# Kernel tuning notes

Measured on AMD Instinct MI355X. Metric: run time of the kernel, lower is better.

Reference implementation:

```python
import jax, jax.numpy as jnp
import numpy as np

GRID = 300  # NaiveFourierKANLayer default gridsize
EPS = 1e-5


def layer_norm(x, w, b):
    mu = jnp.mean(x, axis=-1, keepdims=True)
    var = jnp.var(x, axis=-1, keepdims=True)
    return (x - mu) * jax.lax.rsqrt(var + EPS) * w + b


def fourier_kan(x, coeffs, bias):
    # x: [..., I], coeffs: [2, O, I, G], bias: [1, O]
    shp = x.shape
    I = shp[-1]
    xf = x.reshape(-1, I)
    k = jnp.arange(1, GRID + 1, dtype=x.dtype)           # [G]
    arg = xf[:, :, None] * k                             # [B, I, G]
    y = jnp.einsum('big,oig->bo', jnp.cos(arg), coeffs[0])
    y = y + jnp.einsum('big,oig->bo', jnp.sin(arg), coeffs[1])
    y = y + bias                                         # bias broadcasts [1, O]
    return y.reshape(shp[:-1] + (coeffs.shape[1],))


def setup_inputs() -> dict:
    key = jax.random.key(0)
    ks = jax.random.split(key, 4)
    B, N, D = 8, 196, 128          # batch, in_channels, in_dim
    O1 = 2 * D                     # amplifier out_dim
    x = jax.random.normal(ks[0], (B, N, D), dtype=jnp.float32)
    fc1_coeffs = jax.random.normal(ks[1], (2, O1, D, GRID), dtype=jnp.float32) / np.sqrt(D * GRID)
    fc2_coeffs = jax.random.normal(ks[2], (2, N, N, GRID), dtype=jnp.float32) / np.sqrt(N * GRID)
    return {
        'x': x,
        'ln1_w': jnp.ones((D,), jnp.float32),
        'ln1_b': jnp.zeros((D,), jnp.float32),
        'fc1_coeffs': fc1_coeffs,
        'fc1_bias': jnp.zeros((1, O1), jnp.float32),
        'ln2_w': jnp.ones((O1,), jnp.float32),
        'ln2_b': jnp.zeros((O1,), jnp.float32),
        'fc2_coeffs': fc2_coeffs,
        'fc2_bias': jnp.zeros((1, N), jnp.float32),
    }


def reference(x, ln1_w, ln1_b, fc1_coeffs, fc1_bias, ln2_w, ln2_b, fc2_coeffs, fc2_bias):
    B, N, D = x.shape
    # amplifier: LN over in_dim, FourierKAN in_dim -> 2*in_dim
    h = fourier_kan(layer_norm(x, ln1_w, ln1_b), fc1_coeffs, fc1_bias)   # [B, N, 2D]
    # channel_mix: LN over 2*in_dim, transpose, FourierKAN over channels, transpose back
    h = layer_norm(h, ln2_w, ln2_b)
    h = jnp.transpose(h, (0, 2, 1))                                      # [B, 2D, N]
    h = fourier_kan(h, fc2_coeffs, fc2_bias)                             # [B, 2D, N]
    h = jnp.transpose(h, (0, 2, 1))                                      # [B, N, 2D]
    return h.reshape(-1, 2 * N, D)                                       # [B, 2N, D]
```

## Files before the change

### kernel.cpp

```cpp
#include <hip/hip_runtime.h>
#include <math.h>

typedef short short8 __attribute__((ext_vector_type(8)));
typedef float f32x4 __attribute__((ext_vector_type(4)));

#define EPSF 1e-5f

union FragU { uint4 q; unsigned u[4]; short8 v; };

__device__ __forceinline__ unsigned pack_trunc2(float lo_val, float hi_val) {
    return __builtin_amdgcn_perm(__float_as_uint(hi_val), __float_as_uint(lo_val), 0x07060302u);
}
__device__ __forceinline__ float trunc_bf(float x) {
    return __uint_as_float(__float_as_uint(x) & 0xFFFF0000u);
}

#define LGKM0_BAR() do { \
    asm volatile("s_waitcnt lgkmcnt(0)" ::: "memory"); \
    __builtin_amdgcn_s_barrier(); \
    __builtin_amdgcn_sched_barrier(0); \
    asm volatile("" ::: "memory"); \
} while (0)

__global__ void ln1_kernel(const float* __restrict__ x, const float* __restrict__ w,
                           const float* __restrict__ b, float* __restrict__ xnT) {
    int r = blockIdx.x;
    int t = threadIdx.x;
    const float* row = x + (size_t)r * 128;
    float v0 = row[t], v1 = row[t + 64];
    float s = v0 + v1, q = v0 * v0 + v1 * v1;
    #pragma unroll
    for (int off = 32; off > 0; off >>= 1) {
        s += __shfl_down(s, off);
        q += __shfl_down(q, off);
    }
    s = __shfl(s, 0); q = __shfl(q, 0);
    float mu = s * (1.f / 128.f);
    float var = q * (1.f / 128.f) - mu * mu;
    float rs = rsqrtf(var + EPSF);
    xnT[(size_t)t * 1792 + r]        = (v0 - mu) * rs * w[t]      + b[t];
    xnT[(size_t)(t + 64) * 1792 + r] = (v1 - mu) * rs * w[t + 64] + b[t + 64];
}

__launch_bounds__(256)
__global__ void fc1_kernel(const float* __restrict__ xnT, const float* __restrict__ coeffs,
                           float* __restrict__ h1, int KS) {
    const int nt = blockIdx.x;
    const int mt = blockIdx.y;
    const int ks = blockIdx.z;
    const int i0 = (ks * 128) / KS, i1 = ((ks + 1) * 128) / KS;
    const int t = threadIdx.x;
    const int wv = t >> 6, ln = t & 63;
    const int q = ln >> 4, col = ln & 15;
    const int mwrow = mt * 256 + wv * 64;

    __shared__ unsigned bhi[128 * 36];
    __shared__ unsigned blo[128 * 36];

    const float* c0 = coeffs;
    const float* c1 = coeffs + (size_t)256 * 128 * 300;

    f32x4 acc[4][8] = {};

    const int srow = t >> 1;
    const int j0 = (t & 1) * 16;
    const int og = nt * 128 + srow;
    const size_t prow = (size_t)og * 128;

    for (int i = i0; i < i1; ++i) {
        float zu[4];
        #pragma unroll
        for (int mf = 0; mf < 4; ++mf) {
            int m = mwrow + mf * 16 + col;
            zu[mf] = (m < 1568) ? xnT[(size_t)i * 1792 + m] : 0.f;
        }
        const float* p0 = c0 + (prow + i) * 300;
        const float* p1 = c1 + (prow + i) * 300;

        for (int c = 0; c < 10; ++c) {
            __syncthreads();
            {
                unsigned hw[16], lw[16];
                #pragma unroll
                for (int k4 = 0; k4 < 4; ++k4) {
                    int g = c * 32 + j0 + k4 * 4;
                    float w0[4], w1[4];
                    if (g + 4 <= 300) {
                        float4 a = *(const float4*)(p0 + g);
                        float4 bb = *(const float4*)(p1 + g);
                        w0[0]=a.x; w0[1]=a.y; w0[2]=a.z; w0[3]=a.w;
                        w1[0]=bb.x; w1[1]=bb.y; w1[2]=bb.z; w1[3]=bb.w;
                    } else {
                        #pragma unroll
                        for (int e = 0; e < 4; ++e) {
                            int gg = g + e; bool ok = gg < 300;
                            w0[e] = ok ? p0[gg] : 0.f;
                            w1[e] = ok ? p1[gg] : 0.f;
                        }
                    }
                    #pragma unroll
                    for (int e = 0; e < 4; ++e) {
                        hw[k4*4+e] = pack_trunc2(w0[e], w1[e]);
                        lw[k4*4+e] = pack_trunc2(w0[e]-trunc_bf(w0[e]), w1[e]-trunc_bf(w1[e]));
                    }
                }
                int base = srow * 36 + j0;
                *(uint4*)&bhi[base]      = make_uint4(hw[0], hw[1], hw[2], hw[3]);
                *(uint4*)&bhi[base + 4]  = make_uint4(hw[4], hw[5], hw[6], hw[7]);
                *(uint4*)&bhi[base + 8]  = make_uint4(hw[8], hw[9], hw[10], hw[11]);
                *(uint4*)&bhi[base + 12] = make_uint4(hw[12], hw[13], hw[14], hw[15]);
                *(uint4*)&blo[base]      = make_uint4(lw[0], lw[1], lw[2], lw[3]);
                *(uint4*)&blo[base + 4]  = make_uint4(lw[4], lw[5], lw[6], lw[7]);
                *(uint4*)&blo[base + 8]  = make_uint4(lw[8], lw[9], lw[10], lw[11]);
                *(uint4*)&blo[base + 12] = make_uint4(lw[12], lw[13], lw[14], lw[15]);
            }
            __syncthreads();
            #pragma unroll
            for (int h = 0; h < 2; ++h) {
                FragU ah[4], al[4];
                #pragma unroll
                for (int mf = 0; mf < 4; ++mf) {
                    #pragma unroll
                    for (int d = 0; d < 4; ++d) {
                        float kf = (float)(c * 32 + h * 16 + q * 4 + d + 1);
                        float a = zu[mf] * kf;
                        float cv = __cosf(a), sv = __sinf(a);
                        ah[mf].u[d] = pack_trunc2(cv, sv);
                        al[mf].u[d] = pack_trunc2(cv - trunc_bf(cv), sv - trunc_bf(sv));
                    }
                }
                #pragma unroll
                for (int nf = 0; nf < 8; ++nf) {
                    int addr = (nf * 16 + col) * 36 + h * 16 + q * 4;
                    FragU bh, bl;
                    bh.q = *(const uint4*)&bhi[addr];
                    bl.q = *(const uint4*)&blo[addr];
                    #pragma unroll
                    for (int mf = 0; mf < 4; ++mf) {
                        acc[mf][nf] = __builtin_amdgcn_mfma_f32_16x16x32_bf16(ah[mf].v, bh.v, acc[mf][nf], 0, 0, 0);
                        acc[mf][nf] = __builtin_amdgcn_mfma_f32_16x16x32_bf16(ah[mf].v, bl.v, acc[mf][nf], 0, 0, 0);
                        acc[mf][nf] = __builtin_amdgcn_mfma_f32_16x16x32_bf16(al[mf].v, bh.v, acc[mf][nf], 0, 0, 0);
                    }
                }
            }
        }
    }
    #pragma unroll
    for (int mf = 0; mf < 4; ++mf) {
        if (mwrow + mf * 16 >= 1568) continue;
        int mbase = mwrow + mf * 16 + q * 4;
        #pragma unroll
        for (int nf = 0; nf < 8; ++nf) {
            int o = nt * 128 + nf * 16 + col;
            #pragma unroll
            for (int r = 0; r < 4; ++r)
                atomicAdd(&h1[(size_t)(mbase + r) * 256 + o], acc[mf][nf][r]);
        }
    }
}

__global__ void ln2_kernel(const float* __restrict__ h1, const float* __restrict__ bias,
                           const float* __restrict__ w, const float* __restrict__ b,
                           float* __restrict__ h1n) {
    int r = blockIdx.x;
    int t = threadIdx.x;
    float v = h1[(size_t)r * 256 + t] + bias[t];
    float s = v, q = v * v;
    #pragma unroll
    for (int off = 32; off > 0; off >>= 1) {
        s += __shfl_down(s, off);
        q += __shfl_down(q, off);
    }
    __shared__ float ss[4], qq[4];
    int wid = t >> 6;
    if ((t & 63) == 0) { ss[wid] = s; qq[wid] = q; }
    __syncthreads();
    float S = ss[0] + ss[1] + ss[2] + ss[3];
    float Q = qq[0] + qq[1] + qq[2] + qq[3];
    float mu = S * (1.f / 256.f);
    float var = Q * (1.f / 256.f) - mu * mu;
    float rs = rsqrtf(var + EPSF);
    h1n[(size_t)r * 256 + t] = (v - mu) * rs * w[t] + b[t];
}

__device__ __forceinline__ void cmul(float& xr, float& xi, float br, float bi) {
    float nr = xr * br - xi * bi;
    float ni = xr * bi + xi * br;
    xr = nr; xi = ni;
}

__launch_bounds__(256)
__global__ void fc2_kernel(const float* __restrict__ h1n, const float* __restrict__ coeffs,
                           float* __restrict__ out, int KS) {
    const int nt = blockIdx.x;
    const int b  = blockIdx.y;
    const int ks = blockIdx.z;
    const int i0 = (ks * 196) / KS, i1 = ((ks + 1) * 196) / KS;
    const int t = threadIdx.x;
    const int wv = t >> 6, ln = t & 63;
    const int q = ln >> 4, col = ln & 15;
    const int cwb = wv * 64;

    __shared__ unsigned bs[2][128 * 36];

    const float* d0 = coeffs;
    const float* d1 = coeffs + (size_t)196 * 196 * 300;

    f32x4 acc[4][8] = {};

    const int srow = t >> 1;
    const int j0 = (t & 1) * 16;
    const int og = nt * 128 + srow;
    const bool son = (og < 196);
    const size_t prow = (size_t)og * 196;

    float w0[16], w1[16];

    auto LOAD = [&](int i, int c) {
        const float* p0 = d0 + (prow + i) * 300;
        const float* p1 = d1 + (prow + i) * 300;
        #pragma unroll
        for (int k4 = 0; k4 < 4; ++k4) {
            int g = c * 32 + j0 + k4 * 4;
            if (son && g + 4 <= 300) {
                float4 a  = *(const float4*)(p0 + g);
                float4 bb = *(const float4*)(p1 + g);
                w0[k4*4+0]=a.x;  w0[k4*4+1]=a.y;  w0[k4*4+2]=a.z;  w0[k4*4+3]=a.w;
                w1[k4*4+0]=bb.x; w1[k4*4+1]=bb.y; w1[k4*4+2]=bb.z; w1[k4*4+3]=bb.w;
            } else {
                #pragma unroll
                for (int e = 0; e < 4; ++e) {
                    int gg = g + e; bool ok = son && (gg < 300);
                    w0[k4*4+e] = ok ? p0[gg] : 0.f;
                    w1[k4*4+e] = ok ? p1[gg] : 0.f;
                }
            }
        }
    };

    auto PACKSTORE = [&](int buf) {
        unsigned hw[16];
        #pragma unroll
        for (int e = 0; e < 16; ++e) hw[e] = pack_trunc2(w0[e], w1[e]);
        int base = srow * 36 + j0;
        *(uint4*)&bs[buf][base]      = make_uint4(hw[0],  hw[1],  hw[2],  hw[3]);
        *(uint4*)&bs[buf][base + 4]  = make_uint4(hw[4],  hw[5],  hw[6],  hw[7]);
        *(uint4*)&bs[buf][base + 8]  = make_uint4(hw[8],  hw[9],  hw[10], hw[11]);
        *(uint4*)&bs[buf][base + 12] = make_uint4(hw[12], hw[13], hw[14], hw[15]);
    };

    int cur = 0;
    LOAD(i0, 0);
    for (int i = i0; i < i1; ++i) {
        float Rc[4], Rs[4], E1c[4], E1s[4], E13c[4], E13s[4];
        #pragma unroll
        for (int mf = 0; mf < 4; ++mf) {
            float x = h1n[((size_t)b * 196 + i) * 256 + cwb + mf * 16 + col];
            float c1_ = __cosf(x), s1_ = __sinf(x);
            float c2 = c1_*c1_ - s1_*s1_, s2 = 2.f*c1_*s1_;
            float c4 = c2*c2 - s2*s2,    s4 = 2.f*c2*s2;
            float c8 = c4*c4 - s4*s4,    s8 = 2.f*c4*s4;
            float c12 = c8*c4 - s8*s4,   s12 = c8*s4 + s8*c4;
            float c13 = c12*c1_ - s12*s1_, s13 = c12*s1_ + s12*c1_;
            float rc = c1_, rs = s1_;
            float m4c = (q & 1) ? c4 : 1.f, m4s = (q & 1) ? s4 : 0.f;
            cmul(rc, rs, m4c, m4s);
            float m8c = (q & 2) ? c8 : 1.f, m8s = (q & 2) ? s8 : 0.f;
            cmul(rc, rs, m8c, m8s);
            Rc[mf] = rc; Rs[mf] = rs;
            E1c[mf] = c1_; E1s[mf] = s1_;
            E13c[mf] = c13; E13s[mf] = s13;
        }
        for (int c = 0; c < 10; ++c) {
            PACKSTORE(cur);
            int ni = i, nc = c + 1;
            if (nc == 10) { nc = 0; ni = i + 1; }
            if (ni < i1) LOAD(ni, nc);
            LGKM0_BAR();
            __builtin_amdgcn_s_setprio(1);
            #pragma unroll
            for (int h = 0; h < 2; ++h) {
                FragU af[4];
                #pragma unroll
                for (int mf = 0; mf < 4; ++mf) {
                    #pragma unroll
                    for (int d = 0; d < 4; ++d) {
                        af[mf].u[d] = pack_trunc2(Rc[mf], Rs[mf]);
                        if (d < 3) cmul(Rc[mf], Rs[mf], E1c[mf], E1s[mf]);
                        else       cmul(Rc[mf], Rs[mf], E13c[mf], E13s[mf]);
                    }
                }
                #pragma unroll
                for (int nf = 0; nf < 8; ++nf) {
                    int addr = (nf * 16 + col) * 36 + h * 16 + q * 4;
                    FragU bf;
                    bf.q = *(const uint4*)&bs[cur][addr];
                    #pragma unroll
                    for (int mf = 0; mf < 4; ++mf)
                        acc[mf][nf] = __builtin_amdgcn_mfma_f32_16x16x32_bf16(af[mf].v, bf.v, acc[mf][nf], 0, 0, 0);
                }
            }
            __builtin_amdgcn_s_setprio(0);
            cur ^= 1;
        }
    }
    #pragma unroll
    for (int mf = 0; mf < 4; ++mf) {
        int cbase = cwb + mf * 16 + q * 4;
        #pragma unroll
        for (int nf = 0; nf < 8; ++nf) {
            int o = nt * 128 + nf * 16 + col;
            if (o < 196) {
                #pragma unroll
                for (int r = 0; r < 4; ++r)
                    atomicAdd(&out[((size_t)b * 196 + o) * 256 + cbase + r], acc[mf][nf][r]);
            }
        }
    }
}

__global__ void bias2_kernel(float* __restrict__ out, const float* __restrict__ bias) {
    int idx = blockIdx.x * 256 + threadIdx.x;
    int o = (idx >> 8) % 196;
    out[idx] += bias[o];
}

extern "C" void kernel_launch(void* const* d_in, const int* in_sizes, int n_in,
                              void* d_out, int out_size, void* d_ws, size_t ws_size,
                              hipStream_t stream) {
    const float* x       = (const float*)d_in[0];
    const float* ln1w    = (const float*)d_in[1];
    const float* ln1b    = (const float*)d_in[2];
    const float* fc1c    = (const float*)d_in[3];
    const float* fc1bias = (const float*)d_in[4];
    const float* ln2w    = (const float*)d_in[5];
    const float* ln2b    = (const float*)d_in[6];
    const float* fc2c    = (const float*)d_in[7];
    const float* fc2bias = (const float*)d_in[8];
    float* out = (float*)d_out;

    float* xnT = (float*)d_ws;
    float* h1  = xnT + 229376;
    float* h1n = h1 + 401408;

    hipMemsetAsync(h1, 0, (size_t)401408 * 4, stream);
    hipMemsetAsync(d_out, 0, (size_t)401408 * 4, stream);

    const int ks1 = 32, ks2 = 28;
    ln1_kernel<<<1568, 64, 0, stream>>>(x, ln1w, ln1b, xnT);
    fc1_kernel<<<dim3(2, 7, ks1), 256, 0, stream>>>(xnT, fc1c, h1, ks1);
    ln2_kernel<<<1568, 256, 0, stream>>>(h1, fc1bias, ln2w, ln2b, h1n);
    fc2_kernel<<<dim3(2, 8, ks2), 256, 0, stream>>>(h1n, fc2c, out, ks2);
    bias2_kernel<<<1568, 256, 0, stream>>>(out, fc2bias);
}
```

Before: 842.7 us.

## Stage fc2 coefficients via direct global-to-LDS loads with swizzled layout

Replaces the register-staged load/pack/store of fc2 coefficients with global_load_lds DMA into a swizzled fp32 LDS double buffer, packing to bf16 at fragment-read time. The aim is to free VGPRs and VALU work, allowing two blocks per CU, and to overlap the next chunk's load with the current MFMAs. The last chunk skips its empty half and masks the out-of-range tail. LDS usage doubles because data is kept in fp32, and split-K factors for fc1 and fc2 are also retuned.

```diff
diff --git a/kernel.cpp b/kernel.cpp
--- a/kernel.cpp
+++ b/kernel.cpp
@@ -15,8 +15,14 @@
     return __uint_as_float(__float_as_uint(x) & 0xFFFF0000u);
 }
 
-#define LGKM0_BAR() do { \
-    asm volatile("s_waitcnt lgkmcnt(0)" ::: "memory"); \
+__device__ __forceinline__ void gload16_lds(const void* g, void* l) {
+    __builtin_amdgcn_global_load_lds(
+        (const __attribute__((address_space(1))) void*)g,
+        (__attribute__((address_space(3))) void*)l, 16, 0, 0);
+}
+
+#define PHASE_BAR() do { \
+    asm volatile("s_waitcnt vmcnt(0)" ::: "memory"); \
     __builtin_amdgcn_s_barrier(); \
     __builtin_amdgcn_sched_barrier(0); \
     asm volatile("" ::: "memory"); \
@@ -189,7 +195,7 @@
     xr = nr; xi = ni;
 }
 
-__launch_bounds__(256)
+__launch_bounds__(256, 2)
 __global__ void fc2_kernel(const float* __restrict__ h1n, const float* __restrict__ coeffs,
                            float* __restrict__ out, int KS) {
     const int nt = blockIdx.x;
@@ -201,56 +207,35 @@
     const int q = ln >> 4, col = ln & 15;
     const int cwb = wv * 64;
 
-    __shared__ unsigned bs[2][128 * 36];
+    __shared__ float ldsf[2 * 2 * 4096];
+    char* lds_raw = (char*)&ldsf[0];
 
     const float* d0 = coeffs;
     const float* d1 = coeffs + (size_t)196 * 196 * 300;
 
     f32x4 acc[4][8] = {};
 
-    const int srow = t >> 1;
-    const int j0 = (t & 1) * 16;
-    const int og = nt * 128 + srow;
-    const bool son = (og < 196);
-    const size_t prow = (size_t)og * 196;
-
-    float w0[16], w1[16];
-
-    auto LOAD = [&](int i, int c) {
-        const float* p0 = d0 + (prow + i) * 300;
-        const float* p1 = d1 + (prow + i) * 300;
-        #pragma unroll
-        for (int k4 = 0; k4 < 4; ++k4) {
-            int g = c * 32 + j0 + k4 * 4;
-            if (son && g + 4 <= 300) {
-                float4 a  = *(const float4*)(p0 + g);
-                float4 bb = *(const float4*)(p1 + g);
-                w0[k4*4+0]=a.x;  w0[k4*4+1]=a.y;  w0[k4*4+2]=a.z;  w0[k4*4+3]=a.w;
-                w1[k4*4+0]=bb.x; w1[k4*4+1]=bb.y; w1[k4*4+2]=bb.z; w1[k4*4+3]=bb.w;
-            } else {
-                #pragma unroll
-                for (int e = 0; e < 4; ++e) {
-                    int gg = g + e; bool ok = son && (gg < 300);
-                    w0[k4*4+e] = ok ? p0[gg] : 0.f;
-                    w1[k4*4+e] = ok ? p1[gg] : 0.f;
-                }
-            }
+    const int rb8  = ln >> 3;
+    const int gsub = ((ln & 7) ^ rb8) * 4;
+    const unsigned km = (q == 3) ? 0u : 0xFFFFFFFFu;
+
+    auto STAGE = [&](int i, int c, int buf) {
+        const int g = c * 32 + gsub;
+        const size_t gw = (g + 4 <= 300) ? (size_t)g : 0;
+        #pragma unroll
+        for (int j = 0; j < 4; ++j) {
+            int row = wv * 32 + j * 8 + rb8;
+            int og = nt * 128 + row;
+            if (og > 195) og = 195;
+            size_t go = ((size_t)og * 196 + i) * 300 + gw;
+            unsigned lo = (unsigned)buf * 32768u + (unsigned)wv * 4096u + (unsigned)j * 1024u;
+            gload16_lds(d0 + go, lds_raw + lo);
+            gload16_lds(d1 + go, lds_raw + lo + 16384);
         }
     };
 
-    auto PACKSTORE = [&](int buf) {
-        unsigned hw[16];
-        #pragma unroll
-        for (int e = 0; e < 16; ++e) hw[e] = pack_trunc2(w0[e], w1[e]);
-        int base = srow * 36 + j0;
-        *(uint4*)&bs[buf][base]      = make_uint4(hw[0],  hw[1],  hw[2],  hw[3]);
-        *(uint4*)&bs[buf][base + 4]  = make_uint4(hw[4],  hw[5],  hw[6],  hw[7]);
-        *(uint4*)&bs[buf][base + 8]  = make_uint4(hw[8],  hw[9],  hw[10], hw[11]);
-        *(uint4*)&bs[buf][base + 12] = make_uint4(hw[12], hw[13], hw[14], hw[15]);
-    };
-
     int cur = 0;
-    LOAD(i0, 0);
+    STAGE(i0, 0, 0);
     for (int i = i0; i < i1; ++i) {
         float Rc[4], Rs[4], E1c[4], E1s[4], E13c[4], E13s[4];
         #pragma unroll
@@ -272,14 +257,15 @@
             E13c[mf] = c13; E13s[mf] = s13;
         }
         for (int c = 0; c < 10; ++c) {
-            PACKSTORE(cur);
+            PHASE_BAR();
             int ni = i, nc = c + 1;
             if (nc == 10) { nc = 0; ni = i + 1; }
-            if (ni < i1) LOAD(ni, nc);
-            LGKM0_BAR();
+            if (ni < i1) STAGE(ni, nc, cur ^ 1);
+            __builtin_amdgcn_sched_barrier(0);
             __builtin_amdgcn_s_setprio(1);
             #pragma unroll
             for (int h = 0; h < 2; ++h) {
+                if (h == 1 && c == 9) continue;
                 FragU af[4];
                 #pragma unroll
                 for (int mf = 0; mf < 4; ++mf) {
@@ -292,9 +278,18 @@
                 }
                 #pragma unroll
                 for (int nf = 0; nf < 8; ++nf) {
-                    int addr = (nf * 16 + col) * 36 + h * 16 + q * 4;
+                    int row = nf * 16 + col;
+                    int pb = cur * 32768 + row * 128 + (((h << 6) | (q << 4)) ^ ((col & 7) << 4));
+                    float4 f0 = *(const float4*)(lds_raw + pb);
+                    float4 f1 = *(const float4*)(lds_raw + pb + 16384);
                     FragU bf;
-                    bf.q = *(const uint4*)&bs[cur][addr];
+                    bf.u[0] = pack_trunc2(f0.x, f1.x);
+                    bf.u[1] = pack_trunc2(f0.y, f1.y);
+                    bf.u[2] = pack_trunc2(f0.z, f1.z);
+                    bf.u[3] = pack_trunc2(f0.w, f1.w);
+                    if (c == 9) {
+                        bf.u[0] &= km; bf.u[1] &= km; bf.u[2] &= km; bf.u[3] &= km;
+                    }
                     #pragma unroll
                     for (int mf = 0; mf < 4; ++mf)
                         acc[mf][nf] = __builtin_amdgcn_mfma_f32_16x16x32_bf16(af[mf].v, bf.v, acc[mf][nf], 0, 0, 0);
@@ -346,7 +341,7 @@
     hipMemsetAsync(h1, 0, (size_t)401408 * 4, stream);
     hipMemsetAsync(d_out, 0, (size_t)401408 * 4, stream);
 
-    const int ks1 = 32, ks2 = 28;
+    const int ks1 = 36, ks2 = 32;
     ln1_kernel<<<1568, 64, 0, stream>>>(x, ln1w, ln1b, xnT);
     fc1_kernel<<<dim3(2, 7, ks1), 256, 0, stream>>>(xnT, fc1c, h1, ks1);
     ln2_kernel<<<1568, 256, 0, stream>>>(h1, fc1bias, ln2w, ln2b, h1n);
```

Measured after the change: 689.3 us. -18.2%, faster.
